# Optimization experiments

Hardware: AMD Instinct MI355X
Metric: run time of the kernel (lower is better)

The kernel has to match this reference:

```python
import jax, jax.numpy as jnp
import numpy as np

SEQ = 2048
D_MODEL = 2048
N_HEADS = 16
D_HEAD = D_MODEL // N_HEADS
GN_EPS = 1e-5


def apply_xpos(x, inv=False, base=10000.0, scale_base=512.0):
    # x: (sqlen, d_head). Standard xPos: rotary embedding with exponential length scale.
    s, d = x.shape
    half = d // 2
    freqs = 1.0 / (base ** (jnp.arange(half, dtype=jnp.float32) / half))
    pos = jnp.arange(s, dtype=jnp.float32)
    ang = pos[:, None] * freqs[None, :]                       # (s, half)
    sin, cos = jnp.sin(ang), jnp.cos(ang)
    scale = ((jnp.arange(half, dtype=jnp.float32) + 0.4 * d) / (1.4 * d)) ** (pos[:, None] / scale_base)
    if inv:
        scale = 1.0 / scale
    x1, x2 = x[:, :half], x[:, half:]
    y1 = (x1 * cos - x2 * sin) * scale
    y2 = (x1 * sin + x2 * cos) * scale
    return jnp.concatenate([y1, y2], axis=-1)


def setup_inputs() -> dict:
    key = jax.random.key(0)
    ks = jax.random.split(key, 8)
    s = D_MODEL ** -0.5
    return {
        "x": jax.random.normal(ks[0], (SEQ, D_MODEL), jnp.float32),
        "state": jax.random.normal(ks[1], (N_HEADS, D_HEAD, D_HEAD), jnp.float32) * 0.1,
        "Wqkv": jax.random.normal(ks[2], (3 * D_MODEL, D_MODEL), jnp.float32) * s,
        "Walpha": jax.random.normal(ks[3], (1, D_MODEL), jnp.float32) * s,
        "gn_w": jnp.ones((D_MODEL,), jnp.float32),
        "gn_b": jnp.zeros((D_MODEL,), jnp.float32),
        "Wgate": jax.random.normal(ks[4], (D_MODEL, D_MODEL), jnp.float32) * s,
        "Wout": jax.random.normal(ks[5], (D_MODEL, D_MODEL), jnp.float32) * s,
    }


def reference(x, state, Wqkv, Walpha, gn_w, gn_b, Wgate, Wout):
    sqlen = x.shape[0]
    # qkv projection -> (3, H, s, Dh)
    qkv = (x @ Wqkv.T).reshape(sqlen, 3, N_HEADS, D_HEAD).transpose(1, 2, 0, 3)
    q, k, v = qkv[0], qkv[1], qkv[2]
    q = jax.vmap(apply_xpos)(q)
    k = jax.vmap(lambda t: apply_xpos(t, inv=True))(k)

    alphas = -jnp.log1p(jnp.exp(-(x @ Walpha.T)))             # log-sigmoid, (s, 1)
    k = (1.0 - jnp.exp(alphas)) * k                            # broadcast (s,1) over (H,s,Dh)
    a = jnp.cumsum(alphas, axis=0)                             # (s, 1)

    # Decay matrix; mask BEFORE exp (equivalent to tril-after since upper is zeroed,
    # but avoids overflow in exp for the upper triangle).
    tril = jnp.tril(jnp.ones((sqlen, sqlen), bool))
    Delta = jnp.exp(jnp.where(tril, a - a.T, -jnp.inf))        # (s, s)

    attn = jnp.tril(jnp.einsum('hid,hjd,ij->hij', q, k, Delta))  # (H, s, s)
    ret = jnp.einsum('hij,hjd->ihd', attn, v)                    # (s, H, Dh)

    new_state = jnp.exp(a[-1]) * state                           # (H, Dh, Dh)
    ret = ret + jnp.einsum('hid,hde->ihe', q, new_state)
    new_state = new_state + jnp.einsum('hid,hie,i->hde', k, v, jnp.exp(a[::-1, 0]))

    # GroupNorm(n_heads groups) over d_model, per token
    r = ret.reshape(sqlen, N_HEADS, D_HEAD)
    mu = r.mean(-1, keepdims=True)
    var = r.var(-1, keepdims=True)
    r = (r - mu) * jax.lax.rsqrt(var + GN_EPS)
    ret = r.reshape(sqlen, D_MODEL) * gn_w + gn_b

    gate = jax.nn.swish(ret @ Wgate.T)
    out = (gate * ret) @ Wout.T
    return out, new_state
```

## Files before the change

kernel.cpp:

```cpp
#include <hip/hip_runtime.h>

#define SEQ 2048
#define DM 2048
#define NH 16
#define DH 128

typedef float f32x4 __attribute__((ext_vector_type(4)));
typedef short s16x8 __attribute__((ext_vector_type(8)));

__device__ __forceinline__ ushort f2bf(float f) {
    unsigned u = __builtin_bit_cast(unsigned, f);
    return (ushort)((u + 0x7FFFu + ((u >> 16) & 1u)) >> 16);
}
__device__ __forceinline__ float bf2f(ushort u) {
    return __builtin_bit_cast(float, (unsigned)u << 16);
}
__device__ __forceinline__ void gload_lds16(const void* g, void* l) {
    __builtin_amdgcn_global_load_lds((const __attribute__((address_space(1))) void*)g,
                                     (__attribute__((address_space(3))) void*)l, 16, 0, 0);
}

__global__ __launch_bounds__(256) void k_prep1(const float* __restrict__ x,
                                               const float* __restrict__ wal,
                                               ushort* __restrict__ x_bf,
                                               float* __restrict__ z,
                                               const float* __restrict__ Wqkv,
                                               ushort* __restrict__ Wqkv_bf,
                                               float* __restrict__ tsin,
                                               float* __restrict__ tcos,
                                               float* __restrict__ tsc) {
    int b = blockIdx.x, t = threadIdx.x;
    if (b < SEQ) {
        const float4* xr = (const float4*)(x + (size_t)b * DM);
        const float4* wa = (const float4*)wal;
        float4 v0 = xr[t], v1 = xr[t + 256];
        float4 w0 = wa[t], w1 = wa[t + 256];
        float s = v0.x * w0.x + v0.y * w0.y + v0.z * w0.z + v0.w * w0.w
                + v1.x * w1.x + v1.y * w1.y + v1.z * w1.z + v1.w * w1.w;
        ushort4 o0, o1;
        o0.x = f2bf(v0.x); o0.y = f2bf(v0.y); o0.z = f2bf(v0.z); o0.w = f2bf(v0.w);
        o1.x = f2bf(v1.x); o1.y = f2bf(v1.y); o1.z = f2bf(v1.z); o1.w = f2bf(v1.w);
        ushort4* xb = (ushort4*)(x_bf + (size_t)b * DM);
        xb[t] = o0; xb[t + 256] = o1;
        __shared__ float red[4];
        int lane = t & 63, wv = t >> 6;
        #pragma unroll
        for (int off = 32; off; off >>= 1) s += __shfl_down(s, off);
        if (lane == 0) red[wv] = s;
        __syncthreads();
        if (t == 0) z[b] = red[0] + red[1] + red[2] + red[3];
    } else if (b < SEQ + 3 * DM * DM / 4 / 256) {
        int i = (b - SEQ) * 256 + t;
        float4 v = ((const float4*)Wqkv)[i];
        ushort4 o;
        o.x = f2bf(v.x); o.y = f2bf(v.y); o.z = f2bf(v.z); o.w = f2bf(v.w);
        ((ushort4*)Wqkv_bf)[i] = o;
    } else {
        int idx = (b - SEQ - 3 * DM * DM / 4 / 256) * 256 + t;
        int i = idx >> 6, j = idx & 63;
        float freq = powf(10000.f, -(float)j / 64.f);
        float ang = (float)i * freq;
        tsin[idx] = sinf(ang);
        tcos[idx] = cosf(ang);
        tsc[idx]  = powf(((float)j + 51.2f) / 179.2f, (float)i / 512.f);
    }
}

__global__ __launch_bounds__(256) void k_scan(const float* __restrict__ z,
                                              float* __restrict__ a,
                                              float* __restrict__ wrev,
                                              float* __restrict__ kscale,
                                              float* __restrict__ exp_alast) {
    __shared__ float sh[SEQ];
    __shared__ float csum[256];
    int t = threadIdx.x;
    for (int i = t; i < SEQ; i += 256) {
        float al = -log1pf(expf(-z[i]));
        sh[i] = al;
        kscale[i] = 1.f - expf(al);
    }
    __syncthreads();
    int base = t * 8;
    float run = 0.f, loc[8];
    #pragma unroll
    for (int j = 0; j < 8; j++) { run += sh[base + j]; loc[j] = run; }
    csum[t] = run;
    __syncthreads();
    if (t == 0) {
        float r = 0.f;
        for (int i = 0; i < 256; i++) { float v = csum[i]; csum[i] = r; r += v; }
    }
    __syncthreads();
    float off = csum[t];
    #pragma unroll
    for (int j = 0; j < 8; j++) { float av = loc[j] + off; sh[base + j] = av; a[base + j] = av; }
    __syncthreads();
    for (int i = t; i < SEQ; i += 256) wrev[i] = expf(sh[SEQ - 1 - i]);
    if (t == 0) *exp_alast = expf(sh[SEQ - 1]);
}

template <int EPI, int STORE_BF16>
__global__ __launch_bounds__(256) void k_gemm_mfma(
    const ushort* __restrict__ A,
    const ushort* __restrict__ B,
    void* __restrict__ Cv, int ldc,
    const ushort* __restrict__ aux,
    int K)
{
    __shared__ __align__(16) ushort As[128 * 32];
    __shared__ __align__(16) ushort Bs[128 * 32];
    int bx = blockIdx.x, by = blockIdx.y;
    int nwg = gridDim.x * gridDim.y;
    if ((nwg & 7) == 0) {
        int id = by * gridDim.x + bx;
        int cpx = nwg >> 3;
        int swz = (id & 7) * cpx + (id >> 3);
        bx = swz % gridDim.x; by = swz / gridDim.x;
    }
    int bm = by * 128, bn = bx * 128;
    int tid = threadIdx.x;
    int w = tid >> 6, l = tid & 63;
    int wr = w >> 1, wc = w & 1;
    int lr = l & 15, kg = l >> 4;

    int srow = w * 16 + (l >> 2);
    int scol = (l & 3) * 8;
    const ushort* ga0 = A + (size_t)(bm + srow) * K + scol;
    const ushort* ga1 = A + (size_t)(bm + 64 + srow) * K + scol;
    const ushort* gb0 = B + (size_t)(bn + srow) * K + scol;
    const ushort* gb1 = B + (size_t)(bn + 64 + srow) * K + scol;
    ushort* la0 = As + w * 512;
    ushort* la1 = As + 2048 + w * 512;
    ushort* lb0 = Bs + w * 512;
    ushort* lb1 = Bs + 2048 + w * 512;

    f32x4 acc[4][4] = {};

    for (int k0 = 0; k0 < K; k0 += 32) {
        __syncthreads();
        gload_lds16(ga0 + k0, la0);
        gload_lds16(ga1 + k0, la1);
        gload_lds16(gb0 + k0, lb0);
        gload_lds16(gb1 + k0, lb1);
        __syncthreads();

        s16x8 af[4], bfr[4];
        #pragma unroll
        for (int m = 0; m < 4; m++)
            af[m] = *(const s16x8*)(As + (wr * 64 + m * 16 + lr) * 32 + kg * 8);
        #pragma unroll
        for (int n = 0; n < 4; n++)
            bfr[n] = *(const s16x8*)(Bs + (wc * 64 + n * 16 + lr) * 32 + kg * 8);
        #pragma unroll
        for (int m = 0; m < 4; m++)
            #pragma unroll
            for (int n = 0; n < 4; n++)
                asm volatile("v_mfma_f32_16x16x32_bf16 %0, %1, %2, %0"
                             : "+v"(acc[m][n]) : "v"(af[m]), "v"(bfr[n]));
    }
    asm volatile("s_nop 7\n\ts_nop 7\n\ts_nop 7" ::: );

    #pragma unroll
    for (int m = 0; m < 4; m++) {
        int grow = bm + wr * 64 + m * 16 + kg * 4;
        #pragma unroll
        for (int n = 0; n < 4; n++) {
            int gcol = bn + wc * 64 + n * 16 + lr;
            #pragma unroll
            for (int j = 0; j < 4; j++) {
                float c = acc[m][n][j];
                size_t off = (size_t)(grow + j) * ldc + gcol;
                if (EPI == 1) {
                    float sig = 1.f / (1.f + __expf(-c));
                    c = c * sig * bf2f(aux[off]);
                }
                if (STORE_BF16) ((ushort*)Cv)[off] = f2bf(c);
                else            ((float*)Cv)[off] = c;
            }
        }
    }
}

__global__ __launch_bounds__(256) void k_gemm_qkv(
    const ushort* __restrict__ A,
    const ushort* __restrict__ B,
    const float* __restrict__ tsin,
    const float* __restrict__ tcos,
    const float* __restrict__ tsc,
    const float* __restrict__ kscale,
    const float* __restrict__ wrev,
    ushort* __restrict__ qh,
    ushort* __restrict__ kh,
    ushort* __restrict__ vth,
    ushort* __restrict__ kwtr,
    const float* __restrict__ state,
    const float* __restrict__ exp_alast,
    float* __restrict__ out_state)
{
    if (blockIdx.x == 48) {
        float ea = *exp_alast;
        int idx0 = blockIdx.y * 16384 + threadIdx.x;
        #pragma unroll
        for (int it = 0; it < 16; it++) {
            int idx = idx0 + it * 1024;
            float4 v = ((const float4*)state)[idx / 4 + 0];
            out_state[idx] = state[idx] * ea;
            out_state[idx + 256] = state[idx + 256] * ea;
            out_state[idx + 512] = state[idx + 512] * ea;
            out_state[idx + 768] = state[idx + 768] * ea;
            (void)v;
        }
        return;
    }
    __shared__ __align__(16) char smem[34816];
    ushort* As = (ushort*)smem;
    ushort* Bs = (ushort*)(smem + 8192);
    const int K = DM;
    int bx = blockIdx.x, by = blockIdx.y;
    {
        int id = by * 48 + bx;
        int swz = (id & 7) * 96 + (id >> 3);
        bx = swz % 48; by = swz / 48;
    }
    int bm = by * 128, bn = bx * 128;
    int tid = threadIdx.x;
    int w = tid >> 6, l = tid & 63;
    int wr = w >> 1, wc = w & 1;
    int lr = l & 15, kg = l >> 4;

    int srow = w * 16 + (l >> 2);
    int scol = (l & 3) * 8;
    const ushort* ga0 = A + (size_t)(bm + srow) * K + scol;
    const ushort* ga1 = A + (size_t)(bm + 64 + srow) * K + scol;
    const ushort* gb0 = B + (size_t)(bn + srow) * K + scol;
    const ushort* gb1 = B + (size_t)(bn + 64 + srow) * K + scol;
    ushort* la0 = As + w * 512;
    ushort* la1 = As + 2048 + w * 512;
    ushort* lb0 = Bs + w * 512;
    ushort* lb1 = Bs + 2048 + w * 512;

    f32x4 acc[4][4] = {};

    for (int k0 = 0; k0 < K; k0 += 32) {
        __syncthreads();
        gload_lds16(ga0 + k0, la0);
        gload_lds16(ga1 + k0, la1);
        gload_lds16(gb0 + k0, lb0);
        gload_lds16(gb1 + k0, lb1);
        __syncthreads();

        s16x8 af[4], bfr[4];
        #pragma unroll
        for (int m = 0; m < 4; m++)
            af[m] = *(const s16x8*)(As + (wr * 64 + m * 16 + lr) * 32 + kg * 8);
        #pragma unroll
        for (int n = 0; n < 4; n++)
            bfr[n] = *(const s16x8*)(Bs + (wc * 64 + n * 16 + lr) * 32 + kg * 8);
        #pragma unroll
        for (int m = 0; m < 4; m++)
            #pragma unroll
            for (int n = 0; n < 4; n++)
                asm volatile("v_mfma_f32_16x16x32_bf16 %0, %1, %2, %0"
                             : "+v"(acc[m][n]) : "v"(af[m]), "v"(bfr[n]));
    }
    asm volatile("s_nop 7\n\ts_nop 7\n\ts_nop 7" ::: );

    __syncthreads();
    ushort* S = (ushort*)smem;
    #pragma unroll
    for (int m = 0; m < 4; m++) {
        int row = wr * 64 + m * 16 + kg * 4;
        #pragma unroll
        for (int n = 0; n < 4; n++) {
            int col = wc * 64 + n * 16 + lr;
            #pragma unroll
            for (int j = 0; j < 4; j++)
                S[(row + j) * 129 + col] = f2bf(acc[m][n][j]);
        }
    }
    __syncthreads();

    int type = bn >> 11;
    int h = (bn & 2047) >> 7;

    if (type < 2) {
        #pragma unroll 4
        for (int rr = 0; rr < 32; rr++) {
            int r = w * 32 + rr;
            int i = bm + r;
            float sn = tsin[i * 64 + l], cs = tcos[i * 64 + l], sc = tsc[i * 64 + l];
            float v1 = bf2f(S[r * 129 + l]), v2 = bf2f(S[r * 129 + l + 64]);
            float r1 = v1 * cs - v2 * sn, r2 = v1 * sn + v2 * cs;
            size_t ob = ((size_t)h * SEQ + i) * DH;
            if (type == 0) {
                qh[ob + l]      = f2bf(r1 * sc);
                qh[ob + l + 64] = f2bf(r2 * sc);
            } else {
                float ks = kscale[i], wv = wrev[i];
                float isc = 1.f / sc;
                float k1 = r1 * isc * ks, k2 = r2 * isc * ks;
                kh[ob + l]      = f2bf(k1);
                kh[ob + l + 64] = f2bf(k2);
                S[r * 129 + l]      = f2bf(k1 * wv);
                S[r * 129 + l + 64] = f2bf(k2 * wv);
            }
        }
    }
    if (type >= 1) {
        __syncthreads();
        ushort* dstT = (type == 1) ? kwtr : vth;
        #pragma unroll 4
        for (int dd = 0; dd < 32; dd++) {
            int d = w * 32 + dd;
            ushort2 o;
            o.x = S[(2 * l) * 129 + d];
            o.y = S[(2 * l + 1) * 129 + d];
            *(ushort2*)(dstT + ((size_t)h * DH + d) * SEQ + bm + 2 * l) = o;
        }
    }
}

#define NUNITS 48
__constant__ unsigned char U_QT[NUNITS] = {
    31,31,30,15, 30,29,29,28,14, 28,27,27,26,13, 26,25,25,24,12,
    24,23,23,22,11, 22,21,21,20,10, 20,19,19,18,9, 18,17,17,16,8,
    16,7,6,5,4,3,2,1,0};
__constant__ unsigned char U_T0[NUNITS] = {
    0,16,0,0, 16,0,15,0,0, 15,0,14,0,0, 14,0,13,0,0,
    13,0,12,0,0, 12,0,11,0,0, 11,0,10,0,0, 10,0,9,0,0,
    9,0,0,0,0,0,0,0,0};
__constant__ unsigned char U_T1[NUNITS] = {
    16,32,16,16, 31,15,30,15,15, 29,14,28,14,14, 27,13,26,13,13,
    25,12,24,12,12, 23,11,22,11,11, 21,10,20,10,10, 19,9,18,9,9,
    17,8,7,6,5,4,3,2,1};

__global__ __launch_bounds__(256) void k_attn_mega(
    const ushort* __restrict__ qh,
    const ushort* __restrict__ kh,
    const ushort* __restrict__ vth,
    const ushort* __restrict__ kwtr,
    const float* __restrict__ a,
    float* __restrict__ ret,
    float* __restrict__ ret2,
    float* __restrict__ out_state,
    const float* __restrict__ Wgate,
    ushort* __restrict__ Wgate_bf,
    const float* __restrict__ Wout,
    ushort* __restrict__ Wout_bf)
{
    __shared__ __align__(16) char smem[81920];
    int h = blockIdx.x, u = blockIdx.y;
    int tid = threadIdx.x;
    int w = tid >> 6, l = tid & 63;
    int lr = l & 15, kg = l >> 4;

    if (u >= 56) {
        int id = (u - 56) * NH + h;
        const float4* g0 = (const float4*)Wgate;
        const float4* g1 = (const float4*)Wout;
        #pragma unroll 4
        for (int it = 0; it < 32; it++) {
            int idx = id * 8192 + it * 256 + tid;
            float4 v = g0[idx];
            ushort4 o;
            o.x = f2bf(v.x); o.y = f2bf(v.y); o.z = f2bf(v.z); o.w = f2bf(v.w);
            ((ushort4*)Wgate_bf)[idx] = o;
            v = g1[idx];
            o.x = f2bf(v.x); o.y = f2bf(v.y); o.z = f2bf(v.z); o.w = f2bf(v.w);
            ((ushort4*)Wout_bf)[idx] = o;
        }
        return;
    }
    if (u >= 48) {
        int ch = u - 48;
        const ushort* A = kwtr + (size_t)h * DH * SEQ + ch * (SEQ / 8);
        const ushort* B = vth  + (size_t)h * DH * SEQ + ch * (SEQ / 8);
        ushort* As = (ushort*)smem;
        ushort* Bs = (ushort*)(smem + 8192);
        int wr = w >> 1, wc = w & 1;
        int srow = w * 16 + (l >> 2);
        int scol = (l & 3) * 8;
        const ushort* ga0 = A + (size_t)srow * SEQ + scol;
        const ushort* ga1 = A + (size_t)(64 + srow) * SEQ + scol;
        const ushort* gb0 = B + (size_t)srow * SEQ + scol;
        const ushort* gb1 = B + (size_t)(64 + srow) * SEQ + scol;
        ushort* la0 = As + w * 512;
        ushort* la1 = As + 2048 + w * 512;
        ushort* lb0 = Bs + w * 512;
        ushort* lb1 = Bs + 2048 + w * 512;
        f32x4 acc[4][4] = {};
        for (int k0 = 0; k0 < SEQ / 8; k0 += 32) {
            __syncthreads();
            gload_lds16(ga0 + k0, la0);
            gload_lds16(ga1 + k0, la1);
            gload_lds16(gb0 + k0, lb0);
            gload_lds16(gb1 + k0, lb1);
            __syncthreads();
            s16x8 af[4], bfr[4];
            #pragma unroll
            for (int m = 0; m < 4; m++)
                af[m] = *(const s16x8*)(As + (wr * 64 + m * 16 + lr) * 32 + kg * 8);
            #pragma unroll
            for (int n = 0; n < 4; n++)
                bfr[n] = *(const s16x8*)(Bs + (wc * 64 + n * 16 + lr) * 32 + kg * 8);
            #pragma unroll
            for (int m = 0; m < 4; m++)
                #pragma unroll
                for (int n = 0; n < 4; n++)
                    asm volatile("v_mfma_f32_16x16x32_bf16 %0, %1, %2, %0"
                                 : "+v"(acc[m][n]) : "v"(af[m]), "v"(bfr[n]));
        }
        asm volatile("s_nop 7\n\ts_nop 7\n\ts_nop 7" ::: );
        float* p = out_state + (size_t)h * DH * DH;
        #pragma unroll
        for (int m = 0; m < 4; m++) {
            int grow = wr * 64 + m * 16 + kg * 4;
            #pragma unroll
            for (int n = 0; n < 4; n++) {
                int gcol = wc * 64 + n * 16 + lr;
                #pragma unroll
                for (int j = 0; j < 4; j++)
                    unsafeAtomicAdd(&p[(size_t)(grow + j) * DH + gcol], acc[m][n][j]);
            }
        }
        return;
    }

    int qt = U_QT[u], t0 = U_T0[u], t1 = U_T1[u];
    int i0 = qt * 64;
    const ushort* Q  = qh  + (size_t)h * SEQ * DH;
    const ushort* K  = kh  + (size_t)h * SEQ * DH;
    const ushort* Vt = vth + (size_t)h * DH * SEQ;
#define KS(B) ((ushort*)(smem + (B) * 16384))
#define VS(B) ((ushort*)(smem + 32768 + (B) * 16384))
    char* Ps = smem + 65536;
    float* a_lds = (float*)(smem + 73728);

    int span = t1 * 64;
    for (int i = tid; i < span; i += 256) a_lds[i] = a[i];

    s16x8 qf[4];
    #pragma unroll
    for (int c = 0; c < 4; c++)
        qf[c] = *(const s16x8*)(Q + (size_t)(i0 + w * 16 + lr) * DH + c * 32 + kg * 8);
    float aq[4];
    #pragma unroll
    for (int r = 0; r < 4; r++) aq[r] = a[i0 + w * 16 + kg * 4 + r];

    f32x4 oacc[8] = {};

#define STAGE(T, B) do { int j0_ = (T) * 64;                                      \
    _Pragma("unroll") for (int g = 0; g < 4; g++) {                               \
        int row = w * 16 + g * 4 + (l >> 4);                                      \
        int cb = ((l & 15) * 16) ^ ((row & 7) << 4);                              \
        gload_lds16(K + (size_t)(j0_ + row) * DH + cb / 2,                        \
                    (char*)KS(B) + (w * 16 + g * 4) * 256); }                     \
    _Pragma("unroll") for (int g = 0; g < 4; g++) {                               \
        int e = w * 32 + g * 8 + (l >> 3);                                        \
        int cb = ((l & 7) * 16) ^ ((e & 7) << 4);                                 \
        gload_lds16(Vt + (size_t)e * SEQ + j0_ + cb / 2,                          \
                    (char*)VS(B) + (w * 32 + g * 8) * 128); }                     \
} while (0)

    STAGE(t0, 0);
    __syncthreads();

    for (int t = t0; t < t1; t++) {
        int cur = (t - t0) & 1;
        if (t + 1 < t1) {
            STAGE(t + 1, cur ^ 1);
            asm volatile("s_waitcnt vmcnt(8)" ::: "memory");
        } else {
            asm volatile("s_waitcnt vmcnt(0)" ::: "memory");
        }
        __builtin_amdgcn_s_barrier();

        f32x4 sacc[4] = {};
        __builtin_amdgcn_s_setprio(1);
        #pragma unroll
        for (int n = 0; n < 4; n++) {
            int krow = n * 16 + lr;
            #pragma unroll
            for (int c = 0; c < 4; c++) {
                s16x8 kf = *(const s16x8*)((const char*)KS(cur) + krow * 256 +
                            ((c * 64 + kg * 16) ^ ((krow & 7) << 4)));
                asm volatile("v_mfma_f32_16x16x32_bf16 %0, %1, %2, %0"
                             : "+v"(sacc[n]) : "v"(qf[c]), "v"(kf));
            }
        }
        __builtin_amdgcn_s_setprio(0);
        asm volatile("s_nop 7\n\ts_nop 7" ::: );

        int j0 = t * 64;
        float aref = a_lds[j0];
        float ei[4], ej[4];
        #pragma unroll
        for (int r = 0; r < 4; r++) ei[r] = __expf(aq[r] - aref);
        #pragma unroll
        for (int n = 0; n < 4; n++) ej[n] = __expf(aref - a_lds[j0 + n * 16 + lr]);
        bool diag = (t == qt);
        #pragma unroll
        for (int n = 0; n < 4; n++) {
            #pragma unroll
            for (int r = 0; r < 4; r++) {
                float wv = ei[r] * ej[n];
                if (diag)
                    wv = (n * 16 + lr <= w * 16 + kg * 4 + r) ? wv : 0.f;
                float p = sacc[n][r] * wv;
                int prow = w * 16 + kg * 4 + r;
                *(ushort*)(Ps + prow * 128 +
                           (((n * 16 + lr) * 2) ^ ((prow & 7) << 4))) = f2bf(p);
            }
        }
        __builtin_amdgcn_s_setprio(1);
        #pragma unroll
        for (int c2 = 0; c2 < 2; c2++) {
            int prow = w * 16 + lr;
            s16x8 pf = *(const s16x8*)((const char*)Ps + prow * 128 +
                        ((c2 * 64 + kg * 16) ^ ((prow & 7) << 4)));
            #pragma unroll
            for (int n2 = 0; n2 < 8; n2++) {
                int erow = n2 * 16 + lr;
                s16x8 vf = *(const s16x8*)((const char*)VS(cur) + erow * 128 +
                            ((c2 * 64 + kg * 16) ^ ((erow & 7) << 4)));
                asm volatile("v_mfma_f32_16x16x32_bf16 %0, %1, %2, %0"
                             : "+v"(oacc[n2]) : "v"(pf), "v"(vf));
            }
        }
        __builtin_amdgcn_s_setprio(0);
        asm volatile("s_waitcnt lgkmcnt(0)" ::: "memory");
        __builtin_amdgcn_s_barrier();
    }
#undef STAGE
    asm volatile("s_nop 7\n\ts_nop 7\n\ts_nop 7" ::: );

    float* dst = (t0 == 0) ? ret + (size_t)i0 * DM
                           : ret2 + (size_t)(i0 - 1024) * DM;
    #pragma unroll
    for (int n2 = 0; n2 < 8; n2++) {
        #pragma unroll
        for (int j = 0; j < 4; j++) {
            int ri = w * 16 + kg * 4 + j;
            dst[(size_t)ri * DM + h * DH + n2 * 16 + lr] = oacc[n2][j];
        }
    }
}

__global__ __launch_bounds__(64) void k_gnorm(const float* __restrict__ ret,
                                              const float* __restrict__ ret2,
                                              const float* __restrict__ gw,
                                              const float* __restrict__ gb,
                                              ushort* __restrict__ retn_bf) {
    int i = blockIdx.x, h = blockIdx.y;
    int t = threadIdx.x;
    const float* r = ret + (size_t)i * DM + h * DH;
    float v0 = r[t], v1 = r[t + 64];
    if (i >= 1024) {
        const float* r2 = ret2 + (size_t)(i - 1024) * DM + h * DH;
        v0 += r2[t]; v1 += r2[t + 64];
    }
    float s = v0 + v1, sq = v0 * v0 + v1 * v1;
    #pragma unroll
    for (int off = 32; off; off >>= 1) { s += __shfl_xor(s, off); sq += __shfl_xor(sq, off); }
    float mu = s * (1.f / 128.f);
    float var = sq * (1.f / 128.f) - mu * mu;
    float inv = rsqrtf(var + 1e-5f);
    ushort* o = retn_bf + (size_t)i * DM + h * DH;
    o[t]      = f2bf((v0 - mu) * inv * gw[h * DH + t]      + gb[h * DH + t]);
    o[t + 64] = f2bf((v1 - mu) * inv * gw[h * DH + t + 64] + gb[h * DH + t + 64]);
}

extern "C" void kernel_launch(void* const* d_in, const int* in_sizes, int n_in,
                              void* d_out, int out_size, void* d_ws, size_t ws_size,
                              hipStream_t stream) {
    (void)in_sizes; (void)n_in; (void)out_size; (void)ws_size;
    const float* x      = (const float*)d_in[0];
    const float* state  = (const float*)d_in[1];
    const float* Wqkv   = (const float*)d_in[2];
    const float* Walpha = (const float*)d_in[3];
    const float* gn_w   = (const float*)d_in[4];
    const float* gn_b   = (const float*)d_in[5];
    const float* Wgate  = (const float*)d_in[6];
    const float* Wout   = (const float*)d_in[7];
    float* out       = (float*)d_out;
    float* out_state = out + (size_t)SEQ * DM;

    char* base = (char*)d_ws;
    ushort* x_bf     = (ushort*)base;
    ushort* retn_bf  = (ushort*)base;
    ushort* Wqkv_bf  = (ushort*)(base + 8388608);
    float*  ret      = (float*)(base + 8388608);
    float*  ret2     = (float*)(base + 25165824);
    ushort* qh       = (ushort*)(base + 33554432);
    ushort* kh       = (ushort*)(base + 41943040);
    ushort* vth      = (ushort*)(base + 50331648);
    ushort* kwtr     = (ushort*)(base + 58720256);
    ushort* gr_bf    = (ushort*)(base + 67108864);
    float*  tsin     = (float*)(base + 75497472);
    float*  tcos     = (float*)(base + 75497472 + 524288);
    float*  tsc      = (float*)(base + 75497472 + 1048576);
    ushort* Wgate_bf = (ushort*)(base + 75497472);
    ushort* Wout_bf  = (ushort*)(base + 83886080);
    float*  smalls   = (float*)(base + 92274688);
    float* z = smalls, *a = z + SEQ, *wrev = a + SEQ, *kscale = wrev + SEQ, *exp_alast = kscale + SEQ;

    k_prep1<<<dim3(SEQ + 3 * DM * DM / 4 / 256 + SEQ * 64 / 256), dim3(256), 0, stream>>>(
        x, Walpha, x_bf, z, Wqkv, Wqkv_bf, tsin, tcos, tsc);
    k_scan<<<dim3(1), dim3(256), 0, stream>>>(z, a, wrev, kscale, exp_alast);
    k_gemm_qkv<<<dim3(49, SEQ / 128), dim3(256), 0, stream>>>(
        x_bf, Wqkv_bf, tsin, tcos, tsc, kscale, wrev, qh, kh, vth, kwtr,
        state, exp_alast, out_state);
    k_attn_mega<<<dim3(NH, 64), dim3(256), 0, stream>>>(
        qh, kh, vth, kwtr, a, ret, ret2, out_state,
        Wgate, Wgate_bf, Wout, Wout_bf);
    k_gnorm<<<dim3(SEQ, NH), dim3(64), 0, stream>>>(ret, ret2, gn_w, gn_b, retn_bf);
    k_gemm_mfma<1, 1><<<dim3(DM / 128, SEQ / 128), dim3(256), 0, stream>>>(
        retn_bf, Wgate_bf, gr_bf, DM, retn_bf, DM);
    k_gemm_mfma<0, 0><<<dim3(DM / 128, SEQ / 128), dim3(256), 0, stream>>>(
        gr_bf, Wout_bf, out, DM, nullptr, DM);
}
```

Baseline: 253.6 us.

## Replace atomic state accumulation with per-chunk partials reduced in groupnorm kernel

The state-update blocks in the attention kernel now write their per-chunk results as plain stores into a partial buffer instead of doing float atomic adds into the output state. Extra blocks appended to the groupnorm launch then sum the 8 partials with the decayed initial state and write the final state. This removes atomic contention and drops the extra state-scaling block column from the QKV GEMM, whose swizzle is generalised to the grid size. The cost is extra partial-buffer traffic and a dependency on the workspace reuse (part aliases gr_bf) staying valid.

After: 240.9 us. 1.05x faster.

```diff
diff --git a/kernel.cpp b/kernel.cpp
--- a/kernel.cpp
+++ b/kernel.cpp
@@ -192,35 +192,18 @@
     ushort* __restrict__ qh,
     ushort* __restrict__ kh,
     ushort* __restrict__ vth,
-    ushort* __restrict__ kwtr,
-    const float* __restrict__ state,
-    const float* __restrict__ exp_alast,
-    float* __restrict__ out_state)
+    ushort* __restrict__ kwtr)
 {
-    if (blockIdx.x == 48) {
-        float ea = *exp_alast;
-        int idx0 = blockIdx.y * 16384 + threadIdx.x;
-        #pragma unroll
-        for (int it = 0; it < 16; it++) {
-            int idx = idx0 + it * 1024;
-            float4 v = ((const float4*)state)[idx / 4 + 0];
-            out_state[idx] = state[idx] * ea;
-            out_state[idx + 256] = state[idx + 256] * ea;
-            out_state[idx + 512] = state[idx + 512] * ea;
-            out_state[idx + 768] = state[idx + 768] * ea;
-            (void)v;
-        }
-        return;
-    }
     __shared__ __align__(16) char smem[34816];
     ushort* As = (ushort*)smem;
     ushort* Bs = (ushort*)(smem + 8192);
     const int K = DM;
     int bx = blockIdx.x, by = blockIdx.y;
     {
-        int id = by * 48 + bx;
-        int swz = (id & 7) * 96 + (id >> 3);
-        bx = swz % 48; by = swz / 48;
+        int id = by * gridDim.x + bx;
+        int cpx = (gridDim.x * gridDim.y) >> 3;
+        int swz = (id & 7) * cpx + (id >> 3);
+        bx = swz % gridDim.x; by = swz / gridDim.x;
     }
     int bm = by * 128, bn = bx * 128;
     int tid = threadIdx.x;
@@ -342,7 +325,7 @@
     const float* __restrict__ a,
     float* __restrict__ ret,
     float* __restrict__ ret2,
-    float* __restrict__ out_state,
+    float* __restrict__ part,
     const float* __restrict__ Wgate,
     ushort* __restrict__ Wgate_bf,
     const float* __restrict__ Wout,
@@ -411,7 +394,7 @@
                                  : "+v"(acc[m][n]) : "v"(af[m]), "v"(bfr[n]));
         }
         asm volatile("s_nop 7\n\ts_nop 7\n\ts_nop 7" ::: );
-        float* p = out_state + (size_t)h * DH * DH;
+        float* p = part + ((size_t)ch * NH + h) * DH * DH;
         #pragma unroll
         for (int m = 0; m < 4; m++) {
             int grow = wr * 64 + m * 16 + kg * 4;
@@ -420,7 +403,7 @@
                 int gcol = wc * 64 + n * 16 + lr;
                 #pragma unroll
                 for (int j = 0; j < 4; j++)
-                    unsafeAtomicAdd(&p[(size_t)(grow + j) * DH + gcol], acc[m][n][j]);
+                    p[(size_t)(grow + j) * DH + gcol] = acc[m][n][j];
             }
         }
         return;
@@ -550,9 +533,29 @@
                                               const float* __restrict__ ret2,
                                               const float* __restrict__ gw,
                                               const float* __restrict__ gb,
-                                              ushort* __restrict__ retn_bf) {
+                                              ushort* __restrict__ retn_bf,
+                                              const float* __restrict__ part,
+                                              const float* __restrict__ state,
+                                              const float* __restrict__ exp_alast,
+                                              float* __restrict__ out_state) {
     int i = blockIdx.x, h = blockIdx.y;
     int t = threadIdx.x;
+    if (i >= SEQ) {
+        int bx2 = i - SEQ;
+        int idx4 = bx2 * 64 + t;
+        size_t off = (size_t)h * (DH * DH / 4) + idx4;
+        float ea = *exp_alast;
+        float4 s4 = ((const float4*)state)[off];
+        float4 acc;
+        acc.x = s4.x * ea; acc.y = s4.y * ea; acc.z = s4.z * ea; acc.w = s4.w * ea;
+        #pragma unroll
+        for (int ch = 0; ch < 8; ch++) {
+            float4 p4 = ((const float4*)part)[((size_t)ch * NH) * (DH * DH / 4) + off];
+            acc.x += p4.x; acc.y += p4.y; acc.z += p4.z; acc.w += p4.w;
+        }
+        ((float4*)out_state)[off] = acc;
+        return;
+    }
     const float* r = ret + (size_t)i * DM + h * DH;
     float v0 = r[t], v1 = r[t + 64];
     if (i >= 1024) {
@@ -595,6 +598,7 @@
     ushort* kh       = (ushort*)(base + 41943040);
     ushort* vth      = (ushort*)(base + 50331648);
     ushort* kwtr     = (ushort*)(base + 58720256);
+    float*  part     = (float*)(base + 67108864);
     ushort* gr_bf    = (ushort*)(base + 67108864);
     float*  tsin     = (float*)(base + 75497472);
     float*  tcos     = (float*)(base + 75497472 + 524288);
@@ -607,13 +611,13 @@
     k_prep1<<<dim3(SEQ + 3 * DM * DM / 4 / 256 + SEQ * 64 / 256), dim3(256), 0, stream>>>(
         x, Walpha, x_bf, z, Wqkv, Wqkv_bf, tsin, tcos, tsc);
     k_scan<<<dim3(1), dim3(256), 0, stream>>>(z, a, wrev, kscale, exp_alast);
-    k_gemm_qkv<<<dim3(49, SEQ / 128), dim3(256), 0, stream>>>(
-        x_bf, Wqkv_bf, tsin, tcos, tsc, kscale, wrev, qh, kh, vth, kwtr,
-        state, exp_alast, out_state);
+    k_gemm_qkv<<<dim3(48, SEQ / 128), dim3(256), 0, stream>>>(
+        x_bf, Wqkv_bf, tsin, tcos, tsc, kscale, wrev, qh, kh, vth, kwtr);
     k_attn_mega<<<dim3(NH, 64), dim3(256), 0, stream>>>(
-        qh, kh, vth, kwtr, a, ret, ret2, out_state,
+        qh, kh, vth, kwtr, a, ret, ret2, part,
         Wgate, Wgate_bf, Wout, Wout_bf);
-    k_gnorm<<<dim3(SEQ, NH), dim3(64), 0, stream>>>(ret, ret2, gn_w, gn_b, retn_bf);
+    k_gnorm<<<dim3(SEQ + 64, NH), dim3(64), 0, stream>>>(
+        ret, ret2, gn_w, gn_b, retn_bf, part, state, exp_alast, out_state);
     k_gemm_mfma<1, 1><<<dim3(DM / 128, SEQ / 128), dim3(256), 0, stream>>>(
         retn_bf, Wgate_bf, gr_bf, DM, retn_bf, DM);
     k_gemm_mfma<0, 0><<<dim3(DM / 128, SEQ / 128), dim3(256), 0, stream>>>(
```
